# Kernel tuning notes

Hardware: AMD Instinct MI355X
Metric: run time of the kernel (lower is better)

## Reference

```python
import jax, jax.numpy as jnp
import numpy as np

C = 128      # c_in
H = 4        # no_heads
DH = 32      # c_hidden // no_heads (per-head dim)
INF = 1e9
EPS = 1e-5


def setup_inputs() -> dict:
    key = jax.random.key(0)
    ks = jax.random.split(key, 10)
    B, I, J = 1, 384, 384
    x = jax.random.normal(ks[0], (B, I, J, C), dtype=jnp.float32)
    mask = jnp.ones((B, I, J), dtype=jnp.float32)
    s = 0.02
    return {
        "x": x,
        "mask": mask,
        "ln_w": jnp.ones((C,), jnp.float32),
        "ln_b": jnp.zeros((C,), jnp.float32),
        "w_tri": jax.random.normal(ks[1], (C, H), jnp.float32) * s,   # bias=False
        "wq": jax.random.normal(ks[2], (C, H * DH), jnp.float32) * s,
        "wk": jax.random.normal(ks[3], (C, H * DH), jnp.float32) * s,
        "wv": jax.random.normal(ks[4], (C, H * DH), jnp.float32) * s,
        "wg": jax.random.normal(ks[5], (C, H * DH), jnp.float32) * s,
        "bg": jnp.zeros((H * DH,), jnp.float32),
        "wo": jax.random.normal(ks[6], (H * DH, C), jnp.float32) * s,
        "bo": jnp.zeros((C,), jnp.float32),
    }


def reference(x, mask, ln_w, ln_b, w_tri, wq, wk, wv, wg, bg, wo, bo):
    # starting=True: attend along rows (J axis), no transpose.
    B, I, J, _ = x.shape
    # LayerNorm over channel dim
    mu = jnp.mean(x, axis=-1, keepdims=True)
    var = jnp.mean(jnp.square(x - mu), axis=-1, keepdims=True)
    xn = (x - mu) * jax.lax.rsqrt(var + EPS) * ln_w + ln_b

    # mask bias: [B, I, 1, 1, J]
    mask_bias = (INF * (mask - 1.0))[:, :, None, None, :]
    # triangle bias: linear -> [B, I, J, H] -> permute (2,0,1) -> [B, H, I, J] -> [B, 1, H, I, J]
    tri = jnp.einsum('bijc,ch->bhij', xn, w_tri)[:, None]

    # multi-head attention with gating (OpenFold-style), batch dims (B, I), seq J
    q = jnp.einsum('bijc,cf->bijf', xn, wq).reshape(B, I, J, H, DH)
    k = jnp.einsum('bijc,cf->bijf', xn, wk).reshape(B, I, J, H, DH)
    v = jnp.einsum('bijc,cf->bijf', xn, wv).reshape(B, I, J, H, DH)
    q = q / np.sqrt(DH).astype(np.float32)

    # scores: [B, I, H, Q, K] + mask bias + triangle bias
    scores = jnp.einsum('biqhd,bikhd->bihqk', q, k) + mask_bias + tri
    a = jax.nn.softmax(scores, axis=-1)
    o = jnp.einsum('bihqk,bikhd->biqhd', a, v).reshape(B, I, J, H * DH)

    g = jax.nn.sigmoid(jnp.einsum('bijc,cf->bijf', xn, wg) + bg)
    o = o * g
    out = jnp.einsum('bijf,fc->bijc', o, wo) + bo
    return out
```

## Files before the change

### kernel.cpp

```cpp
#include <hip/hip_runtime.h>
#include <hip/hip_bf16.h>

#define NPOS (384*384)
#define JDIM 384
#define CDIM 128
#define HNUM 4
#define DHD  32

#define LOG2E 1.4426950408889634f

typedef __attribute__((ext_vector_type(8))) short short8;
typedef __attribute__((ext_vector_type(4))) float floatx4;
typedef unsigned short ushort_t;

#if __has_builtin(__builtin_amdgcn_exp2f)
#define EXP2F(x) __builtin_amdgcn_exp2f(x)
#else
#define EXP2F(x) exp2f(x)
#endif

__device__ __forceinline__ float bf2f(unsigned short u){
  unsigned int x = ((unsigned int)u) << 16;
  return __builtin_bit_cast(float, x);
}
__device__ __forceinline__ unsigned short f2bf(float f){
  unsigned int u = __builtin_bit_cast(unsigned int, f);
  u = u + 0x7FFFu + ((u >> 16) & 1u);
  return (unsigned short)(u >> 16);
}
__device__ __forceinline__ unsigned int cvtpk_bf16(float a, float b){
  unsigned int r;
  asm("v_cvt_pk_bf16_f32 %0, %1, %2" : "=v"(r) : "v"(a), "v"(b));
  return r;
}

__global__ __launch_bounds__(256) void ln_tri_kernel(
    const float* __restrict__ x, const float* __restrict__ lnw,
    const float* __restrict__ lnb, const float* __restrict__ wtri,
    ushort_t* __restrict__ xn, float* __restrict__ trip)
{
  int wave = threadIdx.x >> 6, lane = threadIdx.x & 63;
  int pos = blockIdx.x * 4 + wave;
  const float2 xv = *(const float2*)(x + (size_t)pos*CDIM + lane*2);
  float x0 = xv.x, x1 = xv.y;
  float s = x0 + x1, ss = x0*x0 + x1*x1;
  #pragma unroll
  for (int o = 32; o > 0; o >>= 1){ s += __shfl_xor(s, o); ss += __shfl_xor(ss, o); }
  float mu  = s * (1.0f/128.0f);
  float var = ss * (1.0f/128.0f) - mu*mu;
  float rstd = rsqrtf(var + 1e-5f);
  float2 w2 = *(const float2*)(lnw + lane*2);
  float2 b2 = *(const float2*)(lnb + lane*2);
  float n0 = (x0 - mu)*rstd*w2.x + b2.x;
  float n1 = (x1 - mu)*rstd*w2.y + b2.y;
  ushort2 o2; o2.x = f2bf(n0); o2.y = f2bf(n1);
  *(ushort2*)(xn + (size_t)pos*CDIM + lane*2) = o2;
  float4 wt0 = *(const float4*)(wtri + lane*8);
  float4 wt1 = *(const float4*)(wtri + lane*8 + 4);
  float t0 = n0*wt0.x + n1*wt1.x;
  float t1 = n0*wt0.y + n1*wt1.y;
  float t2 = n0*wt0.z + n1*wt1.z;
  float t3 = n0*wt0.w + n1*wt1.w;
  #pragma unroll
  for (int o = 32; o > 0; o >>= 1){
    t0 += __shfl_xor(t0, o); t1 += __shfl_xor(t1, o);
    t2 += __shfl_xor(t2, o); t3 += __shfl_xor(t3, o);
  }
  if (lane == 0){
    int i = pos / JDIM;
    int j = pos - i*JDIM;
    int tp = j*JDIM + i;
    trip[0*NPOS + tp] = t0 * LOG2E;
    trip[1*NPOS + tp] = t1 * LOG2E;
    trip[2*NPOS + tp] = t2 * LOG2E;
    trip[3*NPOS + tp] = t3 * LOG2E;
  }
}

__global__ __launch_bounds__(256) void wt_kernel(
    const float* wq, const float* wk, const float* wv,
    const float* wg, const float* wo, ushort_t* __restrict__ wt)
{
  int mat = blockIdx.x >> 6;
  int idx = ((blockIdx.x & 63) << 8) | threadIdx.x;
  const float* src = (mat==0)?wq:(mat==1)?wk:(mat==2)?wv:(mat==3)?wg:wo;
  int f = idx >> 7, c = idx & 127;
  wt[mat*16384 + idx] = f2bf(src[c*128 + f]);
}

__device__ __forceinline__ void gemm_body(
    const ushort_t* __restrict__ A, const ushort_t* __restrict__ W,
    void* __restrict__ outv, const float* __restrict__ bias,
    int mode, int row0, ushort_t* As, ushort_t* Bs)
{
  int t = threadIdx.x;
  #pragma unroll
  for (int i = 0; i < 8; i++){
    int v = t + i*256;
    int row = v >> 4, c8 = v & 15;
    *(short8*)(As + row*144 + c8*8) = *(const short8*)(A + (size_t)(row0+row)*CDIM + c8*8);
    *(short8*)(Bs + row*144 + c8*8) = *(const short8*)(W + v*8);
  }
  __syncthreads();
  int w = t >> 6, lane = t & 63;
  int wm = (w & 1) * 64, wn = (w >> 1) * 64;
  int m = lane & 15, q4 = lane >> 4;
  floatx4 acc[4][4];
  #pragma unroll
  for (int mi = 0; mi < 4; mi++)
    #pragma unroll
    for (int ni = 0; ni < 4; ni++)
      acc[mi][ni] = (floatx4){0.f, 0.f, 0.f, 0.f};
  #pragma unroll
  for (int k0 = 0; k0 < 128; k0 += 32){
    int koff = k0 + q4*8;
    short8 af[4], bf[4];
    #pragma unroll
    for (int mi = 0; mi < 4; mi++) af[mi] = *(const short8*)(As + (wm + mi*16 + m)*144 + koff);
    #pragma unroll
    for (int ni = 0; ni < 4; ni++) bf[ni] = *(const short8*)(Bs + (wn + ni*16 + m)*144 + koff);
    #pragma unroll
    for (int mi = 0; mi < 4; mi++)
      #pragma unroll
      for (int ni = 0; ni < 4; ni++)
        acc[mi][ni] = __builtin_amdgcn_mfma_f32_16x16x32_bf16(af[mi], bf[ni], acc[mi][ni], 0, 0, 0);
  }
  const float scale = 0.17677669529663687f * LOG2E;
  #pragma unroll
  for (int mi = 0; mi < 4; mi++){
    #pragma unroll
    for (int ni = 0; ni < 4; ni++){
      int col = wn + ni*16 + m;
      float bv = (mode >= 2) ? bias[col] : 0.f;
      #pragma unroll
      for (int r = 0; r < 4; r++){
        float val = acc[mi][ni][r];
        if (mode == 1) val *= scale;
        else if (mode == 2) val = 1.f / (1.f + __expf(-(val + bv)));
        else if (mode == 3) val += bv;
        int row = wm + mi*16 + q4*4 + r;
        size_t oidx = (size_t)(row0+row)*CDIM + col;
        if (mode == 3) ((float*)outv)[oidx] = val;
        else           ((ushort_t*)outv)[oidx] = f2bf(val);
      }
    }
  }
}

__global__ __launch_bounds__(256) void proj_gemm_kernel(
    const ushort_t* __restrict__ xn, const ushort_t* __restrict__ wt,
    ushort_t* __restrict__ outb, const float* __restrict__ bg)
{
  __shared__ __align__(16) ushort_t As[128*144];
  __shared__ __align__(16) ushort_t Bs[128*144];
  int proj = blockIdx.y;
  int mode = (proj == 0) ? 1 : (proj == 3) ? 2 : 0;
  gemm_body(xn, wt + proj*16384, outb + (size_t)proj*NPOS*CDIM, bg, mode,
            blockIdx.x * 128, As, Bs);
}

__global__ __launch_bounds__(256) void out_gemm_kernel(
    const ushort_t* __restrict__ og, const ushort_t* __restrict__ wt,
    float* __restrict__ out, const float* __restrict__ bo)
{
  __shared__ __align__(16) ushort_t As[128*144];
  __shared__ __align__(16) ushort_t Bs[128*144];
  gemm_body(og, wt, (void*)out, bo, 3, blockIdx.x * 128, As, Bs);
}

#define VT_STRIDE 392
#define P_STRIDE  40
__global__ __launch_bounds__(512, 4) void attn_kernel(
    const ushort_t* __restrict__ qb, const ushort_t* __restrict__ kb,
    const ushort_t* __restrict__ vb, const ushort_t* __restrict__ gb,
    const float* __restrict__ mask, const float* __restrict__ trip,
    ushort_t* __restrict__ og)
{
  __shared__ __align__(16) ushort_t Ks[JDIM*32];
  __shared__ __align__(16) ushort_t Vt[32*VT_STRIDE];
  __shared__ __align__(16) ushort_t Pb[8*48*P_STRIDE];
  int i = blockIdx.x, h = blockIdx.y;
  int t = threadIdx.x;
  size_t rbase = (size_t)i * JDIM;

  for (int idx = t; idx < JDIM*4; idx += 512){
    int j = idx >> 2, c8 = idx & 3;
    *(short8*)(Ks + j*32 + c8*8) = *(const short8*)(kb + (rbase + j)*CDIM + h*DHD + c8*8);
    short8 v8 = *(const short8*)(vb + (rbase + j)*CDIM + h*DHD + c8*8);
    int jb = j & 31;
    int jp = (j & ~31) | (((jb & 15) << 1) | (jb >> 4));
    #pragma unroll
    for (int e = 0; e < 8; e++) Vt[(c8*8 + e)*VT_STRIDE + jp] = (unsigned short)v8[e];
  }
  __syncthreads();

  int w = t >> 6, lane = t & 63;
  int m = lane & 15, q4 = lane >> 4;
  int wm = w * 48;
  ushort_t* Pw = Pb + w * 48 * P_STRIDE;

  short8 qf[3];
  #pragma unroll
  for (int t6 = 0; t6 < 3; t6++)
    qf[t6] = *(const short8*)(qb + (rbase + wm + t6*16 + m)*CDIM + h*DHD + q4*8);

  floatx4 oacc[3][2];
  float lpart[3][4];
  #pragma unroll
  for (int t6 = 0; t6 < 3; t6++){
    oacc[t6][0] = (floatx4){0.f,0.f,0.f,0.f};
    oacc[t6][1] = (floatx4){0.f,0.f,0.f,0.f};
    #pragma unroll
    for (int r = 0; r < 4; r++) lpart[t6][r] = 0.f;
  }

  const float* triph = trip + (size_t)h * NPOS;

  for (int kbk = 0; kbk < 12; kbk++){
    int col0 = kbk * 32;
    short8 kf0 = *(const short8*)(Ks + (col0 + m)*32 + q4*8);
    short8 kf1 = *(const short8*)(Ks + (col0 + 16 + m)*32 + q4*8);
    float mb0 = (1e9f*LOG2E) * (mask[rbase + col0 + m] - 1.0f);
    float mb1 = (1e9f*LOG2E) * (mask[rbase + col0 + 16 + m] - 1.0f);

    #pragma unroll
    for (int t6 = 0; t6 < 3; t6++){
      int qrow0 = wm + t6*16 + q4*4;
      float4 tt0 = *(const float4*)(triph + (size_t)(col0 + m)*JDIM + qrow0);
      float4 tt1 = *(const float4*)(triph + (size_t)(col0 + 16 + m)*JDIM + qrow0);
      floatx4 z0 = (floatx4){tt0.x + mb0, tt0.y + mb0, tt0.z + mb0, tt0.w + mb0};
      floatx4 z1 = (floatx4){tt1.x + mb1, tt1.y + mb1, tt1.z + mb1, tt1.w + mb1};
      floatx4 s0 = __builtin_amdgcn_mfma_f32_16x16x32_bf16(qf[t6], kf0, z0, 0, 0, 0);
      floatx4 s1 = __builtin_amdgcn_mfma_f32_16x16x32_bf16(qf[t6], kf1, z1, 0, 0, 0);
      #pragma unroll
      for (int r = 0; r < 4; r++){
        float p0 = EXP2F(s0[r]);
        float p1 = EXP2F(s1[r]);
        lpart[t6][r] += p0 + p1;
        *(unsigned int*)(Pw + (t6*16 + q4*4 + r)*P_STRIDE + m*2) = cvtpk_bf16(p0, p1);
      }
    }
    short8 vf0 = *(const short8*)(Vt + m*VT_STRIDE + col0 + q4*8);
    short8 vf1 = *(const short8*)(Vt + (16 + m)*VT_STRIDE + col0 + q4*8);
    #pragma unroll
    for (int t6 = 0; t6 < 3; t6++){
      short8 pf = *(const short8*)(Pw + (t6*16 + m)*P_STRIDE + q4*8);
      oacc[t6][0] = __builtin_amdgcn_mfma_f32_16x16x32_bf16(pf, vf0, oacc[t6][0], 0, 0, 0);
      oacc[t6][1] = __builtin_amdgcn_mfma_f32_16x16x32_bf16(pf, vf1, oacc[t6][1], 0, 0, 0);
    }
  }

  #pragma unroll
  for (int t6 = 0; t6 < 3; t6++)
    #pragma unroll
    for (int r = 0; r < 4; r++){
      float l = lpart[t6][r];
      l += __shfl_xor(l, 1); l += __shfl_xor(l, 2);
      l += __shfl_xor(l, 4); l += __shfl_xor(l, 8);
      lpart[t6][r] = 1.0f / (l + 1e-30f);
    }

  #pragma unroll
  for (int t6 = 0; t6 < 3; t6++){
    int qrow = wm + t6*16 + q4*4;
    #pragma unroll
    for (int dt = 0; dt < 2; dt++){
      #pragma unroll
      for (int r = 0; r < 4; r++){
        size_t oidx = (rbase + qrow + r)*CDIM + h*DHD + dt*16 + m;
        float o = oacc[t6][dt][r] * lpart[t6][r] * bf2f(gb[oidx]);
        og[oidx] = f2bf(o);
      }
    }
  }
}

extern "C" void kernel_launch(void* const* d_in, const int* in_sizes, int n_in,
                              void* d_out, int out_size, void* d_ws, size_t ws_size,
                              hipStream_t stream)
{
  const float* x    = (const float*)d_in[0];
  const float* mask = (const float*)d_in[1];
  const float* lnw  = (const float*)d_in[2];
  const float* lnb  = (const float*)d_in[3];
  const float* wtri = (const float*)d_in[4];
  const float* wq   = (const float*)d_in[5];
  const float* wk   = (const float*)d_in[6];
  const float* wv   = (const float*)d_in[7];
  const float* wg   = (const float*)d_in[8];
  const float* bg   = (const float*)d_in[9];
  const float* wo   = (const float*)d_in[10];
  const float* bo   = (const float*)d_in[11];

  char* ws = (char*)d_ws;
  const size_t SZ = (size_t)NPOS * CDIM * 2;
  ushort_t* xn  = (ushort_t*)(ws);
  ushort_t* qb  = (ushort_t*)(ws + 1*SZ);
  ushort_t* kbp = (ushort_t*)(ws + 2*SZ);
  ushort_t* vbp = (ushort_t*)(ws + 3*SZ);
  ushort_t* gbp = (ushort_t*)(ws + 4*SZ);
  ushort_t* og  = (ushort_t*)(ws + 5*SZ);
  ushort_t* wt  = (ushort_t*)(ws + 6*SZ);
  float*    tri = (float*)(ws + 6*SZ + 5*16384*2);

  ln_tri_kernel<<<NPOS/4, 256, 0, stream>>>(x, lnw, lnb, wtri, xn, tri);
  wt_kernel<<<320, 256, 0, stream>>>(wq, wk, wv, wg, wo, wt);
  proj_gemm_kernel<<<dim3(NPOS/128, 4), 256, 0, stream>>>(xn, wt, qb, bg);
  attn_kernel<<<dim3(JDIM, HNUM), 512, 0, stream>>>(qb, kbp, vbp, gbp, mask, tri, og);
  out_gemm_kernel<<<NPOS/128, 256, 0, stream>>>(og, wt + 4*16384, (float*)d_out, bo);
}
```

Measured before the change: 391.3 us.

## Compute transposed scores so probabilities stay in registers, drop LDS P buffer

The score MFMA now computes K·Q^T instead of Q·K^T. Each lane then holds probabilities in the layout needed as the A operand of the PV MFMA, so the LDS round-trip through the Pb buffer is removed. The triangle-bias buffer is re-laid out in 4-column groups and the V transpose permutation is changed to match the new fragment order. The K smem stride is padded and the mask is loaded as float4. Row-sum reduction moves to cross-quad shuffles plus a per-row broadcast, which adds a few shuffles in the epilogue.

```diff
diff --git a/kernel.cpp b/kernel.cpp
--- a/kernel.cpp
+++ b/kernel.cpp
@@ -11,6 +11,7 @@
 
 typedef __attribute__((ext_vector_type(8))) short short8;
 typedef __attribute__((ext_vector_type(4))) float floatx4;
+typedef __attribute__((ext_vector_type(4))) unsigned int uintx4;
 typedef unsigned short ushort_t;
 
 #if __has_builtin(__builtin_amdgcn_exp2f)
@@ -69,7 +70,7 @@
   if (lane == 0){
     int i = pos / JDIM;
     int j = pos - i*JDIM;
-    int tp = j*JDIM + i;
+    int tp = (j >> 2)*(JDIM*4) + i*4 + (j & 3);
     trip[0*NPOS + tp] = t0 * LOG2E;
     trip[1*NPOS + tp] = t1 * LOG2E;
     trip[2*NPOS + tp] = t2 * LOG2E;
@@ -168,27 +169,26 @@
   gemm_body(og, wt, (void*)out, bo, 3, blockIdx.x * 128, As, Bs);
 }
 
+#define KS_STRIDE 36
 #define VT_STRIDE 392
-#define P_STRIDE  40
 __global__ __launch_bounds__(512, 4) void attn_kernel(
     const ushort_t* __restrict__ qb, const ushort_t* __restrict__ kb,
     const ushort_t* __restrict__ vb, const ushort_t* __restrict__ gb,
     const float* __restrict__ mask, const float* __restrict__ trip,
     ushort_t* __restrict__ og)
 {
-  __shared__ __align__(16) ushort_t Ks[JDIM*32];
+  __shared__ __align__(16) ushort_t Ks[JDIM*KS_STRIDE];
   __shared__ __align__(16) ushort_t Vt[32*VT_STRIDE];
-  __shared__ __align__(16) ushort_t Pb[8*48*P_STRIDE];
   int i = blockIdx.x, h = blockIdx.y;
   int t = threadIdx.x;
   size_t rbase = (size_t)i * JDIM;
 
   for (int idx = t; idx < JDIM*4; idx += 512){
     int j = idx >> 2, c8 = idx & 3;
-    *(short8*)(Ks + j*32 + c8*8) = *(const short8*)(kb + (rbase + j)*CDIM + h*DHD + c8*8);
+    *(short8*)(Ks + j*KS_STRIDE + c8*8) = *(const short8*)(kb + (rbase + j)*CDIM + h*DHD + c8*8);
     short8 v8 = *(const short8*)(vb + (rbase + j)*CDIM + h*DHD + c8*8);
     int jb = j & 31;
-    int jp = (j & ~31) | (((jb & 15) << 1) | (jb >> 4));
+    int jp = (j & ~31) | (((jb >> 2) & 3)*8 + ((jb >> 4) << 2) + (jb & 3));
     #pragma unroll
     for (int e = 0; e < 8; e++) Vt[(c8*8 + e)*VT_STRIDE + jp] = (unsigned short)v8[e];
   }
@@ -197,7 +197,6 @@
   int w = t >> 6, lane = t & 63;
   int m = lane & 15, q4 = lane >> 4;
   int wm = w * 48;
-  ushort_t* Pw = Pb + w * 48 * P_STRIDE;
 
   short8 qf[3];
   #pragma unroll
@@ -205,70 +204,70 @@
     qf[t6] = *(const short8*)(qb + (rbase + wm + t6*16 + m)*CDIM + h*DHD + q4*8);
 
   floatx4 oacc[3][2];
-  float lpart[3][4];
+  float lsum[3];
   #pragma unroll
   for (int t6 = 0; t6 < 3; t6++){
     oacc[t6][0] = (floatx4){0.f,0.f,0.f,0.f};
     oacc[t6][1] = (floatx4){0.f,0.f,0.f,0.f};
-    #pragma unroll
-    for (int r = 0; r < 4; r++) lpart[t6][r] = 0.f;
+    lsum[t6] = 0.f;
   }
 
   const float* triph = trip + (size_t)h * NPOS;
+  const float MC = 1e9f * LOG2E;
 
   for (int kbk = 0; kbk < 12; kbk++){
     int col0 = kbk * 32;
-    short8 kf0 = *(const short8*)(Ks + (col0 + m)*32 + q4*8);
-    short8 kf1 = *(const short8*)(Ks + (col0 + 16 + m)*32 + q4*8);
-    float mb0 = (1e9f*LOG2E) * (mask[rbase + col0 + m] - 1.0f);
-    float mb1 = (1e9f*LOG2E) * (mask[rbase + col0 + 16 + m] - 1.0f);
-
-    #pragma unroll
-    for (int t6 = 0; t6 < 3; t6++){
-      int qrow0 = wm + t6*16 + q4*4;
-      float4 tt0 = *(const float4*)(triph + (size_t)(col0 + m)*JDIM + qrow0);
-      float4 tt1 = *(const float4*)(triph + (size_t)(col0 + 16 + m)*JDIM + qrow0);
-      floatx4 z0 = (floatx4){tt0.x + mb0, tt0.y + mb0, tt0.z + mb0, tt0.w + mb0};
-      floatx4 z1 = (floatx4){tt1.x + mb1, tt1.y + mb1, tt1.z + mb1, tt1.w + mb1};
-      floatx4 s0 = __builtin_amdgcn_mfma_f32_16x16x32_bf16(qf[t6], kf0, z0, 0, 0, 0);
-      floatx4 s1 = __builtin_amdgcn_mfma_f32_16x16x32_bf16(qf[t6], kf1, z1, 0, 0, 0);
-      #pragma unroll
-      for (int r = 0; r < 4; r++){
-        float p0 = EXP2F(s0[r]);
-        float p1 = EXP2F(s1[r]);
-        lpart[t6][r] += p0 + p1;
-        *(unsigned int*)(Pw + (t6*16 + q4*4 + r)*P_STRIDE + m*2) = cvtpk_bf16(p0, p1);
-      }
-    }
+    short8 kf0 = *(const short8*)(Ks + (col0 + m)*KS_STRIDE + q4*8);
+    short8 kf1 = *(const short8*)(Ks + (col0 + 16 + m)*KS_STRIDE + q4*8);
+    float4 mk0 = *(const float4*)(mask + rbase + col0 + q4*4);
+    float4 mk1 = *(const float4*)(mask + rbase + col0 + 16 + q4*4);
+    float mb0[4] = {(mk0.x-1.f)*MC, (mk0.y-1.f)*MC, (mk0.z-1.f)*MC, (mk0.w-1.f)*MC};
+    float mb1[4] = {(mk1.x-1.f)*MC, (mk1.y-1.f)*MC, (mk1.z-1.f)*MC, (mk1.w-1.f)*MC};
     short8 vf0 = *(const short8*)(Vt + m*VT_STRIDE + col0 + q4*8);
     short8 vf1 = *(const short8*)(Vt + (16 + m)*VT_STRIDE + col0 + q4*8);
+
+    const float* tb0 = triph + (size_t)(kbk*8 + q4)*(JDIM*4);
+    const float* tb1 = triph + (size_t)(kbk*8 + 4 + q4)*(JDIM*4);
+
     #pragma unroll
     for (int t6 = 0; t6 < 3; t6++){
-      short8 pf = *(const short8*)(Pw + (t6*16 + m)*P_STRIDE + q4*8);
+      int q0t = wm + t6*16;
+      float4 tt0 = *(const float4*)(tb0 + (q0t + m)*4);
+      float4 tt1 = *(const float4*)(tb1 + (q0t + m)*4);
+      floatx4 z0 = (floatx4){tt0.x + mb0[0], tt0.y + mb0[1], tt0.z + mb0[2], tt0.w + mb0[3]};
+      floatx4 z1 = (floatx4){tt1.x + mb1[0], tt1.y + mb1[1], tt1.z + mb1[2], tt1.w + mb1[3]};
+      floatx4 s0 = __builtin_amdgcn_mfma_f32_16x16x32_bf16(kf0, qf[t6], z0, 0, 0, 0);
+      floatx4 s1 = __builtin_amdgcn_mfma_f32_16x16x32_bf16(kf1, qf[t6], z1, 0, 0, 0);
+      float p0 = EXP2F(s0[0]), p1 = EXP2F(s0[1]), p2 = EXP2F(s0[2]), p3 = EXP2F(s0[3]);
+      float p4 = EXP2F(s1[0]), p5 = EXP2F(s1[1]), p6 = EXP2F(s1[2]), p7 = EXP2F(s1[3]);
+      lsum[t6] += ((p0 + p1) + (p2 + p3)) + ((p4 + p5) + (p6 + p7));
+      uintx4 pk = (uintx4){cvtpk_bf16(p0, p1), cvtpk_bf16(p2, p3),
+                           cvtpk_bf16(p4, p5), cvtpk_bf16(p6, p7)};
+      short8 pf = __builtin_bit_cast(short8, pk);
       oacc[t6][0] = __builtin_amdgcn_mfma_f32_16x16x32_bf16(pf, vf0, oacc[t6][0], 0, 0, 0);
       oacc[t6][1] = __builtin_amdgcn_mfma_f32_16x16x32_bf16(pf, vf1, oacc[t6][1], 0, 0, 0);
     }
   }
 
-  #pragma unroll
-  for (int t6 = 0; t6 < 3; t6++)
+  float lrec[3];
+  #pragma unroll
+  for (int t6 = 0; t6 < 3; t6++){
+    float l = lsum[t6];
+    l += __shfl_xor(l, 16);
+    l += __shfl_xor(l, 32);
+    lrec[t6] = 1.0f / (l + 1e-30f);
+  }
+
+  #pragma unroll
+  for (int t6 = 0; t6 < 3; t6++){
     #pragma unroll
     for (int r = 0; r < 4; r++){
-      float l = lpart[t6][r];
-      l += __shfl_xor(l, 1); l += __shfl_xor(l, 2);
-      l += __shfl_xor(l, 4); l += __shfl_xor(l, 8);
-      lpart[t6][r] = 1.0f / (l + 1e-30f);
-    }
-
-  #pragma unroll
-  for (int t6 = 0; t6 < 3; t6++){
-    int qrow = wm + t6*16 + q4*4;
-    #pragma unroll
-    for (int dt = 0; dt < 2; dt++){
+      float lrq = __shfl(lrec[t6], (q4 << 2) + r);
+      int qrow = wm + t6*16 + q4*4 + r;
       #pragma unroll
-      for (int r = 0; r < 4; r++){
-        size_t oidx = (rbase + qrow + r)*CDIM + h*DHD + dt*16 + m;
-        float o = oacc[t6][dt][r] * lpart[t6][r] * bf2f(gb[oidx]);
+      for (int dt = 0; dt < 2; dt++){
+        size_t oidx = (rbase + qrow)*CDIM + h*DHD + dt*16 + m;
+        float o = oacc[t6][dt][r] * lrq * bf2f(gb[oidx]);
         og[oidx] = f2bf(o);
       }
     }
```

Measured after the change: 338.2 us. 1.16x faster.
